# Performance work log

Hardware: AMD Instinct MI355X
Metric: run time of the kernel (lower is better)

The kernel has to match this reference:

```python
import jax, jax.numpy as jnp
import numpy as np

DIM = 512
HEADS = 8
DIM_HEAD = 64
LANDMARKS = 256  # dim // 2
PINV_ITERS = 6
KERNEL = 33  # residual conv kernel
NUM_LAYERS = 2
NUM_CLASSES = 2


def layernorm(x, g, b, eps=1e-5):
    mu = x.mean(-1, keepdims=True)
    var = ((x - mu) ** 2).mean(-1, keepdims=True)
    return (x - mu) * jax.lax.rsqrt(var + eps) * g + b


def moore_penrose_pinv(x, iters=PINV_ITERS):
    # x: (b, h, m, m); scaling uses GLOBAL max over all batch/heads (torch.max)
    abs_x = jnp.abs(x)
    col = abs_x.sum(-1).max()
    row = abs_x.sum(-2).max()
    z = jnp.swapaxes(x, -1, -2) / (col * row)
    I = jnp.eye(x.shape[-1], dtype=x.dtype)
    for _ in range(iters):
        xz = x @ z
        z = 0.25 * z @ (13. * I - xz @ (15. * I - xz @ (7. * I - xz)))
    return z


def nystrom_attention(x, w_qkv, w_out, b_out, conv_w):
    # x: (b, n, dim)
    b, n, _ = x.shape
    m = LANDMARKS
    pad = (m - n % m) % m
    if pad:
        x = jnp.pad(x, ((0, 0), (pad, 0), (0, 0)))  # pad at FRONT
    nf = n + pad
    qkv = x @ w_qkv  # (b, nf, 3*h*dh)
    qkv = qkv.reshape(b, nf, 3, HEADS, DIM_HEAD)
    q = jnp.transpose(qkv[:, :, 0], (0, 2, 1, 3)) * (DIM_HEAD ** -0.5)  # (b,h,nf,dh)
    k = jnp.transpose(qkv[:, :, 1], (0, 2, 1, 3))
    v = jnp.transpose(qkv[:, :, 2], (0, 2, 1, 3))
    l = nf // m
    q_l = q.reshape(b, HEADS, m, l, DIM_HEAD).mean(3)  # (b,h,m,dh)
    k_l = k.reshape(b, HEADS, m, l, DIM_HEAD).mean(3)
    sim1 = jnp.einsum('bhid,bhjd->bhij', q, k_l)      # (b,h,nf,m)
    sim2 = jnp.einsum('bhid,bhjd->bhij', q_l, k_l)    # (b,h,m,m)
    sim3 = jnp.einsum('bhid,bhjd->bhij', q_l, k)      # (b,h,m,nf)
    attn1 = jax.nn.softmax(sim1, axis=-1)
    attn2 = jax.nn.softmax(sim2, axis=-1)
    attn3 = jax.nn.softmax(sim3, axis=-1)
    attn2_inv = moore_penrose_pinv(attn2)
    out = (attn1 @ attn2_inv) @ (attn3 @ v)  # (b,h,nf,dh)
    # residual depthwise conv over sequence dim, per head (Conv2d groups=heads)
    res = jax.lax.conv_general_dilated(
        v, conv_w, window_strides=(1, 1), padding=((KERNEL // 2, KERNEL // 2), (0, 0)),
        dimension_numbers=('NCHW', 'OIHW', 'NCHW'), feature_group_count=HEADS)
    out = out + res
    out = jnp.transpose(out, (0, 2, 1, 3)).reshape(b, nf, HEADS * DIM_HEAD)
    out = out @ w_out + b_out
    return out[:, -n:]


def setup_inputs() -> dict:
    key = jax.random.key(0)
    ks = jax.random.split(key, 16)
    B, N = 2, 8191
    s = 0.02
    inp = {
        'h': jax.random.normal(ks[0], (B, N, 1024), jnp.float32),
        'w1': jax.random.normal(ks[1], (1024, DIM), jnp.float32) * s,
        'b1': jnp.zeros((DIM,), jnp.float32),
        'cls_token': jax.random.normal(ks[2], (1, 1, DIM), jnp.float32),
        'ln_g': jnp.ones((NUM_LAYERS, DIM), jnp.float32),
        'ln_b': jnp.zeros((NUM_LAYERS, DIM), jnp.float32),
        'w_qkv': jax.random.normal(ks[3], (NUM_LAYERS, DIM, 3 * HEADS * DIM_HEAD), jnp.float32) * s,
        'w_out': jax.random.normal(ks[4], (NUM_LAYERS, HEADS * DIM_HEAD, DIM), jnp.float32) * s,
        'b_out': jnp.zeros((NUM_LAYERS, DIM), jnp.float32),
        'conv_w': jax.random.normal(ks[5], (NUM_LAYERS, HEADS, 1, KERNEL, 1), jnp.float32) * s,
        'fn_g': jnp.ones((DIM,), jnp.float32),
        'fn_b': jnp.zeros((DIM,), jnp.float32),
        'w2': jax.random.normal(ks[6], (DIM, NUM_CLASSES), jnp.float32) * s,
        'b2': jnp.zeros((NUM_CLASSES,), jnp.float32),
    }
    return inp


def reference(h, w1, b1, cls_token, ln_g, ln_b, w_qkv, w_out, b_out, conv_w, fn_g, fn_b, w2, b2):
    x = jax.nn.relu(h @ w1 + b1)  # (B,N,512)
    B = x.shape[0]
    cls = jnp.broadcast_to(cls_token, (B, 1, DIM))
    x = jnp.concatenate([cls, x], axis=1)  # (B, N+1, 512)
    for i in range(NUM_LAYERS):
        x = x + nystrom_attention(layernorm(x, ln_g[i], ln_b[i]), w_qkv[i], w_out[i], b_out[i], conv_w[i])
    x = layernorm(x, fn_g, fn_b)[:, 0]
    logits = x @ w2 + b2
    return logits
```

## Files before the change

### kernel.cpp

```cpp
#include <hip/hip_runtime.h>
#include <hip/hip_bf16.h>

#define DIM 512
#define HEADS 8
#define DH 64
#define LM 256
#define NF 8192
#define BHN 16

typedef __attribute__((ext_vector_type(8))) short short8;
typedef __attribute__((ext_vector_type(4))) float f32x4;

__device__ __forceinline__ float bf2f(unsigned short u) {
  return __uint_as_float((unsigned)u << 16);
}
__device__ __forceinline__ unsigned short f2bf(float x) {
  unsigned u = __float_as_uint(x);
  unsigned r = u + 0x7fffu + ((u >> 16) & 1u);
  return (unsigned short)(r >> 16);
}

__device__ __forceinline__ void gl2lds16(const void* g, void* l) {
  __builtin_amdgcn_global_load_lds(
      (const __attribute__((address_space(1))) void*)g,
      (__attribute__((address_space(3))) void*)l, 16, 0, 0);
}

__device__ __forceinline__ void lds_fence() {
  asm volatile("s_waitcnt lgkmcnt(0)" ::: "memory");
  __builtin_amdgcn_sched_barrier(0);
}

__device__ __forceinline__ float waveReduceSum(float v) {
#pragma unroll
  for (int o = 1; o < 64; o <<= 1) v += __shfl_xor(v, o);
  return v;
}
__device__ __forceinline__ float waveReduceMax(float v) {
#pragma unroll
  for (int o = 1; o < 64; o <<= 1) v = fmaxf(v, __shfl_xor(v, o));
  return v;
}
__device__ __forceinline__ float blockReduceSum256(float v, float* sm) {
  v = waveReduceSum(v);
  int w = threadIdx.x >> 6;
  __syncthreads();
  if ((threadIdx.x & 63) == 0) sm[w] = v;
  __syncthreads();
  return sm[0] + sm[1] + sm[2] + sm[3];
}
__device__ __forceinline__ float blockReduceMax256(float v, float* sm) {
  v = waveReduceMax(v);
  int w = threadIdx.x >> 6;
  __syncthreads();
  if ((threadIdx.x & 63) == 0) sm[w] = v;
  __syncthreads();
  return fmaxf(fmaxf(sm[0], sm[1]), fmaxf(sm[2], sm[3]));
}

__global__ __launch_bounds__(256)
void cvt_bf16(const float* __restrict__ in, unsigned short* __restrict__ out,
              long long n) {
  long long i = ((long long)blockIdx.x * 256 + threadIdx.x) * 4;
  if (i + 3 < n) {
    float4 v = *(const float4*)&in[i];
    ushort4 o;
    o.x = f2bf(v.x); o.y = f2bf(v.y); o.z = f2bf(v.z); o.w = f2bf(v.w);
    *(ushort4*)&out[i] = o;
  } else {
    for (; i < n; i++) out[i] = f2bf(in[i]);
  }
}

__global__ __launch_bounds__(256)
void cvt_transpose(const float* __restrict__ in, unsigned short* __restrict__ out,
                   int Kd, int Nd) {
  __shared__ float t[32][33];
  int x = threadIdx.x & 31, y = threadIdx.x >> 5;
#pragma unroll
  for (int i = 0; i < 32; i += 8) {
    int k = blockIdx.y * 32 + y + i, n = blockIdx.x * 32 + x;
    t[y + i][x] = in[(long long)k * Nd + n];
  }
  __syncthreads();
#pragma unroll
  for (int i = 0; i < 32; i += 8) {
    int n = blockIdx.x * 32 + y + i, k = blockIdx.y * 32 + x;
    out[(long long)n * Kd + k] = f2bf(t[x][y + i]);
  }
}

__global__ __launch_bounds__(256)
void vt_transpose(const unsigned short* __restrict__ VB,
                  unsigned short* __restrict__ VT) {
  __shared__ unsigned short t[64][80];
  int bh = blockIdx.x >> 7, tile = blockIdx.x & 127;
  int n0 = tile * 64;
  int tid = threadIdx.x;
#pragma unroll
  for (int it = 0; it < 2; it++) {
    int s = it * 256 + tid;
    int nl = s >> 3, sg = s & 7;
    *(short8*)&t[nl][sg * 8] =
        *(const short8*)&VB[((long long)bh * NF + n0 + nl) * DH + sg * 8];
  }
  __syncthreads();
#pragma unroll
  for (int it = 0; it < 2; it++) {
    int s = it * 256 + tid;
    int dl = s >> 3, sg = s & 7;
    short8 v;
#pragma unroll
    for (int j = 0; j < 8; j++) ((unsigned short*)&v)[j] = t[sg * 8 + j][dl];
    *(short8*)&VT[((long long)bh * DH + dl) * NF + n0 + sg * 8] = v;
  }
}

__global__ __launch_bounds__(256) void write_cls(const float* __restrict__ cls,
                                                 float* __restrict__ X) {
  int t = blockIdx.x * 256 + threadIdx.x;
  int b = t >> 9, c = t & 511;
  X[(long long)b * NF * DIM + c] = cls[c];
}

#define MG_RELU 1
#define MG_ADDC 2
#define MG_BIAS 4
__global__ __launch_bounds__(256)
void gemm_mfma(const unsigned short* __restrict__ A,
               const unsigned short* __restrict__ B,
               const float* __restrict__ bias, float* __restrict__ C,
               unsigned short* __restrict__ qkv, unsigned short* __restrict__ vbuf,
               int M, int N, int K, int flags, int remap) {
  __shared__ short8 smem[3072];
  const int tid = threadIdx.x;
  const int lane = tid & 63, wave = tid >> 6;
  const int wm = wave >> 1, wn = wave & 1;
  const int nwg = gridDim.x * gridDim.y;
  const int orig = blockIdx.y * gridDim.x + blockIdx.x;
  const int swz = ((nwg & 7) == 0) ? (orig & 7) * (nwg >> 3) + (orig >> 3) : orig;
  const int m0 = (swz / gridDim.x) * 128, n0 = (swz % gridDim.x) * 128;
  const int r16 = lane & 15, quad = lane >> 4;
  const unsigned short* pa0 = A + (long long)(m0 + 32 * wave + r16) * K + quad * 8;
  const unsigned short* pa1 = A + (long long)(m0 + 32 * wave + 16 + r16) * K + quad * 8;
  const unsigned short* pb0 = B + (long long)(n0 + 32 * wave + r16) * K + quad * 8;
  const unsigned short* pb1 = B + (long long)(n0 + 32 * wave + 16 + r16) * K + quad * 8;
  auto stage = [&](int bsel) {
    short8 (*Als)[64] = (short8 (*)[64])(smem + bsel * 1024);
    short8 (*Bls)[64] = (short8 (*)[64])(smem + bsel * 1024 + 512);
    gl2lds16(pa0, &Als[2 * wave][0]);
    gl2lds16(pa1, &Als[2 * wave + 1][0]);
    gl2lds16(pb0, &Bls[2 * wave][0]);
    gl2lds16(pb1, &Bls[2 * wave + 1][0]);
    pa0 += 32; pa1 += 32; pb0 += 32; pb1 += 32;
  };
  f32x4 acc[4][4] = {};
  const int nsteps = K >> 5;
  stage(0);
  stage(1);
  asm volatile("s_waitcnt vmcnt(4)" ::: "memory");
  __builtin_amdgcn_sched_barrier(0);
  __builtin_amdgcn_s_barrier();
  for (int t = 0; t < nsteps; t++) {
    if (t + 2 < nsteps) stage((t + 2) % 3);
    short8 (*Als)[64] = (short8 (*)[64])(smem + (t % 3) * 1024);
    short8 (*Bls)[64] = (short8 (*)[64])(smem + (t % 3) * 1024 + 512);
    short8 af[4], bfr[4];
#pragma unroll
    for (int mt = 0; mt < 4; mt++) af[mt] = Als[wm * 4 + mt][lane];
#pragma unroll
    for (int nt = 0; nt < 4; nt++) bfr[nt] = Bls[wn * 4 + nt][lane];
#pragma unroll
    for (int mt = 0; mt < 4; mt++)
#pragma unroll
      for (int nt = 0; nt < 4; nt++)
        acc[mt][nt] = __builtin_amdgcn_mfma_f32_16x16x32_bf16(
            af[mt], bfr[nt], acc[mt][nt], 0, 0, 0);
    if (t + 2 < nsteps) {
      asm volatile("s_waitcnt vmcnt(4)" ::: "memory");
    } else {
      asm volatile("s_waitcnt vmcnt(0)" ::: "memory");
    }
    __builtin_amdgcn_sched_barrier(0);
    __builtin_amdgcn_s_barrier();
  }
  if (remap == 2) {
    unsigned short (*Ep)[32][64] = (unsigned short (*)[32][64])smem;
    int gn_base = n0 + wn * 64;
    int s = gn_base >> 9, hh = (gn_base >> 6) & 7;
    float scale = (s == 0) ? 0.125f : 1.f;
    unsigned short* basep =
        (s == 0) ? qkv : (s == 1) ? qkv + (long long)BHN * NF * DH : vbuf;
#pragma unroll
    for (int half = 0; half < 2; half++) {
      lds_fence();
#pragma unroll
      for (int mt = half * 2; mt < half * 2 + 2; mt++)
#pragma unroll
        for (int nt = 0; nt < 4; nt++)
#pragma unroll
          for (int r = 0; r < 4; r++)
            Ep[wave][(mt & 1) * 16 + quad * 4 + r][nt * 16 + r16] =
                f2bf(acc[mt][nt][r] * scale);
      lds_fence();
#pragma unroll
      for (int it = 0; it < 4; it++) {
        int idx = it * 64 + lane;
        int m_l = idx >> 3, sg = idx & 7;
        int gm = m0 + wm * 64 + half * 32 + m_l;
        int b = gm >> 13, n = gm & (NF - 1);
        int bh = b * HEADS + hh;
        short8 v = *(short8*)&Ep[wave][m_l][sg * 8];
        *(short8*)&basep[((long long)bh * NF + n) * DH + sg * 8] = v;
      }
    }
  } else {
#pragma unroll
    for (int mt = 0; mt < 4; mt++) {
#pragma unroll
      for (int nt = 0; nt < 4; nt++) {
#pragma unroll
        for (int r = 0; r < 4; r++) {
          int gm = m0 + wm * 64 + mt * 16 + quad * 4 + r;
          int gn = n0 + wn * 64 + nt * 16 + r16;
          if (gm >= M) continue;
          float v = acc[mt][nt][r];
          if (flags & MG_BIAS) v += bias[gn];
          long long idx;
          if (remap == 1) {
            int b = gm / 8191;
            int n = gm - b * 8191;
            idx = ((long long)(b * NF + 1 + n)) * DIM + gn;
          } else {
            idx = (long long)gm * N + gn;
          }
          if (flags & MG_ADDC) v += C[idx];
          if (flags & MG_RELU) v = fmaxf(v, 0.f);
          C[idx] = v;
        }
      }
    }
  }
}

__global__ __launch_bounds__(512)
void flash_attn1(const unsigned short* __restrict__ QB,
                 const unsigned short* __restrict__ KLB,
                 const unsigned short* __restrict__ WmB,
                 const unsigned short* __restrict__ XNC,
                 unsigned short* __restrict__ XNB2) {
  __shared__ unsigned short Klds[LM * DH];
  __shared__ unsigned short Wlds[DH * LM];
  __shared__ unsigned short Plds[8][16][136];
  const int bh = blockIdx.y, b = bh >> 3, hh = bh & 7;
  const int tid = threadIdx.x, lane = tid & 63, wave = tid >> 6;
  const int r16 = lane & 15, quad = lane >> 4;
  const unsigned short* Aq = QB + (long long)bh * NF * DH;
  const unsigned short* Kg = KLB + (long long)bh * LM * DH;
  const unsigned short* Wg = WmB + (long long)bh * DH * LM;
#pragma unroll
  for (int j = 0; j < 4; j++) {
    int u = j * 8 + wave;
    int s = u * 64 + lane;
    int row = s >> 3, ck = s & 7;
    gl2lds16(Kg + row * DH + ((ck ^ (row & 7)) << 3), (char*)Klds + u * 1024);
  }
#pragma unroll
  for (int j = 0; j < 4; j++) {
    int u = j * 8 + wave;
    int s = u * 64 + lane;
    int row = s >> 5, ck = s & 31;
    gl2lds16(Wg + row * LM + ((ck ^ (row & 7)) << 3), (char*)Wlds + u * 1024);
  }
  __syncthreads();
  short8 ones;
#pragma unroll
  for (int j = 0; j < 8; j++) ((unsigned short*)&ones)[j] = 0x3F80;
#pragma unroll
  for (int rt = 0; rt < 2; rt++) {
    const int m0w = blockIdx.x * 256 + (wave * 2 + rt) * 16;
    short8 af[2];
#pragma unroll
    for (int kc = 0; kc < 2; kc++)
      af[kc] = *(const short8*)&Aq[(long long)(m0w + r16) * DH + kc * 32 + quad * 8];
    f32x4 O[4] = {};
    f32x4 Ls = {};
#pragma unroll
    for (int t = 0; t < 2; t++) {
      int c0 = t * 128;
      f32x4 S[8] = {};
      __builtin_amdgcn_s_setprio(1);
#pragma unroll
      for (int nt = 0; nt < 8; nt++) {
        int kl = c0 + nt * 16 + r16;
#pragma unroll
        for (int kc = 0; kc < 2; kc++) {
          short8 bb = *(const short8*)((const char*)Klds + kl * 128 +
                                       (((kc * 4 + quad) ^ (kl & 7)) << 4));
          S[nt] = __builtin_amdgcn_mfma_f32_16x16x32_bf16(af[kc], bb, S[nt], 0, 0, 0);
        }
      }
      __builtin_amdgcn_s_setprio(0);
#pragma unroll
      for (int nt = 0; nt < 8; nt++)
#pragma unroll
        for (int r = 0; r < 4; r++)
          Plds[wave][quad * 4 + r][nt * 16 + r16] = f2bf(__expf(S[nt][r]));
      lds_fence();
      __builtin_amdgcn_s_setprio(1);
#pragma unroll
      for (int kc = 0; kc < 4; kc++) {
        short8 a = *(short8*)&Plds[wave][r16][kc * 32 + quad * 8];
        Ls = __builtin_amdgcn_mfma_f32_16x16x32_bf16(a, ones, Ls, 0, 0, 0);
#pragma unroll
        for (int nt2 = 0; nt2 < 4; nt2++) {
          int wrow = nt2 * 16 + r16;
          int cu = (c0 >> 3) + kc * 4 + quad;
          short8 bb = *(const short8*)((const char*)Wlds + wrow * 512 +
                                       ((cu ^ (wrow & 7)) << 4));
          O[nt2] = __builtin_amdgcn_mfma_f32_16x16x32_bf16(a, bb, O[nt2], 0, 0, 0);
        }
      }
      __builtin_amdgcn_s_setprio(0);
    }
    float invl[4];
#pragma unroll
    for (int r = 0; r < 4; r++) invl[r] = 1.f / Ls[r];
#pragma unroll
    for (int nt2 = 0; nt2 < 4; nt2++)
#pragma unroll
      for (int r = 0; r < 4; r++) {
        int row = m0w + quad * 4 + r;
        int d = nt2 * 16 + r16;
        long long gi = ((long long)(b * NF + row)) * DIM + hh * DH + d;
        XNB2[gi] = f2bf(O[nt2][r] * invl[r] + bf2f(XNC[gi]));
      }
  }
}

__device__ __forceinline__ void stage_kv3(const unsigned short* Kg,
                                          const unsigned short* Vg,
                                          unsigned short* Kb, unsigned short* Vb,
                                          int kv0, int wave, int lane) {
#pragma unroll
  for (int j = 0; j < 2; j++) {
    int u = j * 8 + wave;
    int s = u * 64 + lane;
    int kr = s >> 3, kc = s & 7;
    gl2lds16(Kg + (long long)(kv0 + kr) * DH + ((kc ^ (kr & 7)) << 3),
             (char*)Kb + u * 1024);
    int vr = s >> 4, vc = s & 15;
    gl2lds16(Vg + (long long)vr * NF + kv0 + ((vc ^ (vr & 7)) << 3),
             (char*)Vb + u * 1024);
  }
}

__global__ __launch_bounds__(512)
void flash_attn3(const unsigned short* __restrict__ QLB,
                 const unsigned short* __restrict__ KB,
                 const unsigned short* __restrict__ VT,
                 float* __restrict__ Opart, float* __restrict__ Lpart) {
  __shared__ unsigned short Klds[2][128 * DH];
  __shared__ unsigned short Vlds[2][DH * 128];
  __shared__ unsigned short Plds[8][16][136];
  const int ks = blockIdx.x, bh = blockIdx.y;
  const int tid = threadIdx.x, lane = tid & 63, wave = tid >> 6;
  const int r16 = lane & 15, quad = lane >> 4;
  const unsigned short* Aq = QLB + (long long)bh * LM * DH;
  const unsigned short* Kg = KB + (long long)bh * NF * DH;
  const unsigned short* Vg = VT + (long long)bh * DH * NF;
  short8 af2[2][2];
#pragma unroll
  for (int rt = 0; rt < 2; rt++) {
    int m0w = (wave * 2 + rt) * 16;
#pragma unroll
    for (int kc = 0; kc < 2; kc++)
      af2[rt][kc] =
          *(const short8*)&Aq[(long long)(m0w + r16) * DH + kc * 32 + quad * 8];
  }
  short8 ones;
#pragma unroll
  for (int j = 0; j < 8; j++) ((unsigned short*)&ones)[j] = 0x3F80;
  f32x4 O2[2][4] = {};
  f32x4 Ls2[2] = {};
  stage_kv3(Kg, Vg, Klds[0], Vlds[0], ks * 512, wave, lane);
  __syncthreads();
  for (int t = 0; t < 4; t++) {
    int cb = t & 1;
    if (t < 3)
      stage_kv3(Kg, Vg, Klds[cb ^ 1], Vlds[cb ^ 1], ks * 512 + (t + 1) * 128,
                wave, lane);
    const unsigned short* Kb = Klds[cb];
    const unsigned short* Vb = Vlds[cb];
#pragma unroll
    for (int rt = 0; rt < 2; rt++) {
      f32x4 S[8] = {};
      __builtin_amdgcn_s_setprio(1);
#pragma unroll
      for (int nt = 0; nt < 8; nt++) {
        int kl = nt * 16 + r16;
#pragma unroll
        for (int kc = 0; kc < 2; kc++) {
          short8 bb = *(const short8*)((const char*)Kb + kl * 128 +
                                       (((kc * 4 + quad) ^ (kl & 7)) << 4));
          S[nt] = __builtin_amdgcn_mfma_f32_16x16x32_bf16(af2[rt][kc], bb, S[nt],
                                                          0, 0, 0);
        }
      }
      __builtin_amdgcn_s_setprio(0);
#pragma unroll
      for (int nt = 0; nt < 8; nt++)
#pragma unroll
        for (int r = 0; r < 4; r++)
          Plds[wave][quad * 4 + r][nt * 16 + r16] = f2bf(__expf(S[nt][r]));
      lds_fence();
      __builtin_amdgcn_s_setprio(1);
#pragma unroll
      for (int kc2 = 0; kc2 < 4; kc2++) {
        short8 a = *(short8*)&Plds[wave][r16][kc2 * 32 + quad * 8];
        Ls2[rt] = __builtin_amdgcn_mfma_f32_16x16x32_bf16(a, ones, Ls2[rt], 0, 0, 0);
#pragma unroll
        for (int nt2 = 0; nt2 < 4; nt2++) {
          int vr = nt2 * 16 + r16;
          int u = kc2 * 4 + quad;
          short8 bb = *(const short8*)((const char*)Vb + vr * 256 +
                                       ((u ^ (vr & 7)) << 4));
          O2[rt][nt2] = __builtin_amdgcn_mfma_f32_16x16x32_bf16(a, bb, O2[rt][nt2],
                                                                0, 0, 0);
        }
      }
      __builtin_amdgcn_s_setprio(0);
    }
    __syncthreads();
  }
  float* Ob = Opart + (((long long)ks * BHN + bh) * LM) * DH;
#pragma unroll
  for (int rt = 0; rt < 2; rt++) {
    int m0w = (wave * 2 + rt) * 16;
#pragma unroll
    for (int nt2 = 0; nt2 < 4; nt2++)
#pragma unroll
      for (int r = 0; r < 4; r++)
        Ob[(long long)(m0w + quad * 4 + r) * DH + nt2 * 16 + r16] = O2[rt][nt2][r];
    if (r16 == 0)
#pragma unroll
      for (int r = 0; r < 4; r++)
        Lpart[((long long)ks * BHN + bh) * LM + m0w + quad * 4 + r] = Ls2[rt][r];
  }
}

__global__ __launch_bounds__(256)
void attn3_merge(const float* __restrict__ Opart, const float* __restrict__ Lpart,
                 float* __restrict__ O3) {
  int idx = blockIdx.x * 256 + threadIdx.x;
  int bh = idx >> 14, rem = idx & 16383;
  int row = rem >> 6, d = rem & 63;
  float L = 0.f, acc = 0.f;
#pragma unroll
  for (int c = 0; c < 16; c++) {
    L += Lpart[((long long)c * BHN + bh) * LM + row];
    acc += Opart[(((long long)c * BHN + bh) * LM + row) * DH + d];
  }
  O3[((long long)bh * LM + row) * DH + d] = acc / L;
}

__global__ __launch_bounds__(256)
void zinit(const float* __restrict__ a2, const unsigned* __restrict__ red,
           unsigned short* __restrict__ zn, unsigned short* __restrict__ zt) {
  float scale = 1.0f / __uint_as_float(red[1]);
  long long idx = (long long)blockIdx.x * 256 + threadIdx.x;
  int bh = (int)(idx >> 16);
  int ij = (int)(idx & 65535);
  int i = ij >> 8, j = ij & 255;
  zn[idx] = f2bf(a2[((long long)bh << 16) + (j << 8) + i] * scale);
  zt[idx] = f2bf(a2[idx] * scale);
}

#define PV_CN 1
#define PV_CT 2
#define PV_CF 4
#define PV_ID 8
__global__ __launch_bounds__(256)
void pinv_bf(const unsigned short* __restrict__ An,
             const unsigned short* __restrict__ Bt,
             unsigned short* __restrict__ Cn, unsigned short* __restrict__ Ct,
             float* __restrict__ Cf, float alpha, float ident, float beta,
             int flags) {
  __shared__ unsigned short Als[32][256];
  __shared__ unsigned short Bls[32][256];
  const int batch = blockIdx.z;
  An += (long long)batch * 65536;
  Bt += (long long)batch * 65536;
  const int tid = threadIdx.x, lane = tid & 63, wave = tid >> 6;
  const int wm2 = wave >> 1, wn2 = wave & 1;
  const int m0 = blockIdx.y * 32, n0 = blockIdx.x * 32;
  const int r16 = lane & 15, quad = lane >> 4;
#pragma unroll
  for (int j = 0; j < 4; j++) {
    int g = (j * 4 + wave) * 64 + lane;
    int row = g >> 5, plog = (g & 31) ^ (row & 7);
    gl2lds16(An + ((m0 + row) << 8) + plog * 8,
             (char*)Als + (j * 4 + wave) * 1024);
    gl2lds16(Bt + ((n0 + row) << 8) + plog * 8,
             (char*)Bls + (j * 4 + wave) * 1024);
  }
  __syncthreads();
  f32x4 acc = {};
  const int arow = wm2 * 16 + r16, brow = wn2 * 16 + r16;
#pragma unroll
  for (int kk = 0; kk < 8; kk++) {
    short8 af = *(const short8*)((const char*)Als + arow * 512 +
                                 ((kk * 4 + quad) ^ (arow & 7)) * 16);
    short8 bfr = *(const short8*)((const char*)Bls + brow * 512 +
                                  ((kk * 4 + quad) ^ (brow & 7)) * 16);
    acc = __builtin_amdgcn_mfma_f32_16x16x32_bf16(af, bfr, acc, 0, 0, 0);
  }
  long long cb = (long long)batch * 65536;
  int ncol = n0 + wn2 * 16 + r16;
  float vals[4];
#pragma unroll
  for (int r = 0; r < 4; r++) {
    int mrow = wm2 * 16 + quad * 4 + r;
    float v = beta * acc[r];
    if (flags & PV_ID) {
      unsigned short a = *(const unsigned short*)(
          (const char*)Als + mrow * 512 +
          (((ncol >> 3) ^ (mrow & 7)) * 16) + (ncol & 7) * 2);
      v += ident * bf2f(a);
    }
    vals[r] = v * alpha;
    int gm = m0 + mrow;
    if (flags & PV_CN) Cn[cb + ((long long)gm << 8) + ncol] = f2bf(vals[r]);
    if (flags & PV_CF) Cf[cb + ((long long)gm << 8) + ncol] = vals[r];
  }
  if (flags & PV_CT) {
    ushort4 o;
    o.x = f2bf(vals[0]); o.y = f2bf(vals[1]);
    o.z = f2bf(vals[2]); o.w = f2bf(vals[3]);
    *(ushort4*)&Ct[cb + ((long long)ncol << 8) + m0 + wm2 * 16 + quad * 4] = o;
  }
}

#define BG_BIDENT 16
__global__ __launch_bounds__(256)
void bgemm(const float* __restrict__ A, const float* __restrict__ B,
           float* __restrict__ C, int M, int N, int K,
           long long sA, long long sB, long long sC,
           float alpha, float ident, int flags) {
  const int batch = blockIdx.z;
  A += (long long)batch * sA;
  B += (long long)batch * sB;
  float* Cb = C + (long long)batch * sC;
  __shared__ float As[16][68];
  __shared__ float Bs[16][68];
  const int tid = threadIdx.x;
  const int tx = tid & 15, ty = tid >> 4;
  const int m0 = blockIdx.y * 64, n0 = blockIdx.x * 64;
  float acc[4][4] = {};
  for (int k0 = 0; k0 < K; k0 += 16) {
    {
      int k = tid & 15;
      int mBase = tid >> 4;
#pragma unroll
      for (int i = 0; i < 4; i++) {
        int m = mBase + i * 16;
        int gm = m0 + m;
        As[k][m] = (gm < M) ? A[(long long)gm * K + (k0 + k)] : 0.f;
      }
    }
    {
      int n = tid & 63;
      int kBase = tid >> 6;
#pragma unroll
      for (int i = 0; i < 4; i++) {
        int k = kBase + i * 4;
        int gn = n0 + n;
        float vb = (gn < N) ? B[(long long)(k0 + k) * N + gn] : 0.f;
        if (flags & BG_BIDENT) vb = ident * ((k0 + k) == gn ? 1.f : 0.f) - vb;
        Bs[k][n] = vb;
      }
    }
    __syncthreads();
#pragma unroll
    for (int k = 0; k < 16; k++) {
      float a[4], b[4];
#pragma unroll
      for (int i = 0; i < 4; i++) a[i] = As[k][ty * 4 + i];
#pragma unroll
      for (int j = 0; j < 4; j++) b[j] = Bs[k][tx * 4 + j];
#pragma unroll
      for (int i = 0; i < 4; i++)
#pragma unroll
        for (int j = 0; j < 4; j++) acc[i][j] = fmaf(a[i], b[j], acc[i][j]);
    }
    __syncthreads();
  }
#pragma unroll
  for (int i = 0; i < 4; i++) {
    int gm = m0 + ty * 4 + i;
    if (gm >= M) continue;
#pragma unroll
    for (int j = 0; j < 4; j++) {
      int gn = n0 + tx * 4 + j;
      if (gn >= N) continue;
      Cb[(long long)gm * N + gn] = alpha * acc[i][j];
    }
  }
}

__global__ __launch_bounds__(256)
void wm_gemm(const float* __restrict__ Z, const float* __restrict__ O3,
             unsigned short* __restrict__ WmT) {
  const int batch = blockIdx.y;
  const int m0 = blockIdx.x * 64;
  const float* A = Z + (long long)batch * 65536;
  const float* B = O3 + (long long)batch * LM * DH;
  __shared__ float As[16][68];
  __shared__ float Bs[16][68];
  const int tid = threadIdx.x, tx = tid & 15, ty = tid >> 4;
  float acc[4][4] = {};
  for (int k0 = 0; k0 < 256; k0 += 16) {
    {
      int k = tid & 15, mB = tid >> 4;
#pragma unroll
      for (int i = 0; i < 4; i++) {
        int m = mB + i * 16;
        As[k][m] = A[(long long)(m0 + m) * 256 + k0 + k];
      }
    }
    {
      int n = tid & 63, kB = tid >> 6;
#pragma unroll
      for (int i = 0; i < 4; i++) {
        int k = kB + i * 4;
        Bs[k][n] = B[(long long)(k0 + k) * DH + n];
      }
    }
    __syncthreads();
#pragma unroll
    for (int k = 0; k < 16; k++) {
      float a[4], b[4];
#pragma unroll
      for (int i = 0; i < 4; i++) a[i] = As[k][ty * 4 + i];
#pragma unroll
      for (int j = 0; j < 4; j++) b[j] = Bs[k][tx * 4 + j];
#pragma unroll
      for (int i = 0; i < 4; i++)
#pragma unroll
        for (int j = 0; j < 4; j++) acc[i][j] = fmaf(a[i], b[j], acc[i][j]);
    }
    __syncthreads();
  }
#pragma unroll
  for (int i = 0; i < 4; i++)
#pragma unroll
    for (int j = 0; j < 4; j++)
      WmT[((long long)batch * DH + tx * 4 + j) * LM + m0 + ty * 4 + i] =
          f2bf(acc[i][j]);
}

__global__ __launch_bounds__(256)
void layernorm_rows_bf16(const float* __restrict__ X, const float* __restrict__ g,
                         const float* __restrict__ bt,
                         unsigned short* __restrict__ Y) {
  __shared__ float sm[4];
  long long r = blockIdx.x;
  const float* x = X + r * DIM;
  int t = threadIdx.x;
  float v0 = x[t], v1 = x[t + 256];
  float mu = blockReduceSum256(v0 + v1, sm) * (1.f / DIM);
  float d0 = v0 - mu, d1 = v1 - mu;
  float var = blockReduceSum256(d0 * d0 + d1 * d1, sm) * (1.f / DIM);
  float rs = 1.0f / sqrtf(var + 1e-5f);
  unsigned short* y = Y + r * DIM;
  y[t] = f2bf(d0 * rs * g[t] + bt[t]);
  y[t + 256] = f2bf(d1 * rs * g[t + 256] + bt[t + 256]);
}

__global__ __launch_bounds__(64)
void landmarks_k(const unsigned short* __restrict__ q,
                 const unsigned short* __restrict__ k,
                 float* __restrict__ ql, float* __restrict__ kl,
                 unsigned short* __restrict__ qlb,
                 unsigned short* __restrict__ klb) {
  int bh = blockIdx.x >> 8, i = blockIdx.x & 255, d = threadIdx.x;
  long long base = ((long long)bh * NF + i * 32) * DH + d;
  float sq = 0.f, sk = 0.f;
#pragma unroll 4
  for (int l = 0; l < 32; l++) {
    sq += bf2f(q[base + (long long)l * DH]);
    sk += bf2f(k[base + (long long)l * DH]);
  }
  long long o = ((long long)bh * LM + i) * DH + d;
  float mq = sq * (1.f / 32.f), mk = sk * (1.f / 32.f);
  ql[o] = mq; kl[o] = mk;
  qlb[o] = f2bf(mq); klb[o] = f2bf(mk);
}

__global__ __launch_bounds__(256)
void sim2_softmax(const float* __restrict__ ql, const float* __restrict__ kl,
                  float* __restrict__ a2, unsigned short* __restrict__ a2b) {
  __shared__ float qs[64];
  __shared__ float sm[4];
  int bh = blockIdx.x >> 8, i = blockIdx.x & 255, t = threadIdx.x;
  if (t < 64) qs[t] = ql[((long long)bh * LM + i) * DH + t];
  __syncthreads();
  const float* krow = kl + (long long)bh * LM * DH + (long long)t * DH;
  float s = 0.f;
#pragma unroll
  for (int d = 0; d < 64; d++) s += qs[d] * krow[d];
  float m = blockReduceMax256(s, sm);
  float e = expf(s - m);
  float sum = blockReduceSum256(e, sm);
  long long off = ((long long)bh * LM + i) * LM + t;
  float v = e / sum;
  a2[off] = v;
  a2b[off] = f2bf(v);
}

__global__ __launch_bounds__(256)
void pinv_reduce(const float* __restrict__ a2, unsigned* __restrict__ red) {
  __shared__ float sm[4];
  int bh = blockIdx.x, t = threadIdx.x;
  const float* A = a2 + (long long)bh * LM * LM;
  float cs = 0.f;
  for (int i = 0; i < 256; i++) cs += fabsf(A[i * 256 + t]);
  float cm = blockReduceMax256(cs, sm);
  if (t == 0) atomicMax(&red[1], __float_as_uint(cm));
}

__global__ __launch_bounds__(256)
void conv_res_bf16(const unsigned short* __restrict__ vt,
                   const float* __restrict__ cw,
                   unsigned short* __restrict__ out) {
  int bh = blockIdx.x >> 6, tile = blockIdx.x & 63;
  int b = bh >> 3, hh = bh & 7;
  int t = threadIdx.x;
  int d = t & 63, pg = t >> 6;
  float wr[33];
#pragma unroll
  for (int kk = 0; kk < 33; kk++) wr[kk] = cw[hh * 33 + kk];
  const unsigned short* src = &vt[((long long)bh * DH + d) * NF];
  int base = tile * 128 + pg * 32;
  int n0 = base - 16;
  float win[64];
#pragma unroll
  for (int jj = 0; jj < 8; jj++) {
    int c = n0 + jj * 8;
    if (c >= 0 && c + 7 < NF) {
      short8 v = *(const short8*)&src[c];
#pragma unroll
      for (int j = 0; j < 8; j++)
        win[jj * 8 + j] = bf2f((unsigned short)v[j]);
    } else {
#pragma unroll
      for (int j = 0; j < 8; j++) {
        int nn = c + j;
        win[jj * 8 + j] = (nn >= 0 && nn < NF) ? bf2f(src[nn]) : 0.f;
      }
    }
  }
  unsigned short* dst = &out[((long long)(b * NF + base)) * DIM + hh * DH + d];
#pragma unroll
  for (int p = 0; p < 32; p++) {
    float s = 0.f;
#pragma unroll
    for (int kk = 0; kk < 33; kk++) s = fmaf(wr[kk], win[p + kk], s);
    dst[(long long)p * DIM] = f2bf(s);
  }
}

__global__ __launch_bounds__(256)
void final_head(const float* __restrict__ X, const float* __restrict__ g,
                const float* __restrict__ bt, const float* __restrict__ w2,
                const float* __restrict__ b2, float* __restrict__ out) {
  __shared__ float sm[4];
  int b = blockIdx.x, t = threadIdx.x;
  const float* row = X + (long long)b * NF * DIM;
  float v0 = row[t], v1 = row[t + 256];
  float mu = blockReduceSum256(v0 + v1, sm) * (1.f / DIM);
  float d0 = v0 - mu, d1 = v1 - mu;
  float var = blockReduceSum256(d0 * d0 + d1 * d1, sm) * (1.f / DIM);
  float rs = 1.0f / sqrtf(var + 1e-5f);
  float y0 = d0 * rs * g[t] + bt[t];
  float y1 = d1 * rs * g[t + 256] + bt[t + 256];
  float l0 = y0 * w2[t * 2 + 0] + y1 * w2[(t + 256) * 2 + 0];
  float l1 = y0 * w2[t * 2 + 1] + y1 * w2[(t + 256) * 2 + 1];
  l0 = blockReduceSum256(l0, sm);
  l1 = blockReduceSum256(l1, sm);
  if (t == 0) {
    out[b * 2 + 0] = l0 + b2[0];
    out[b * 2 + 1] = l1 + b2[1];
  }
}

extern "C" void kernel_launch(void* const* d_in, const int* in_sizes, int n_in,
                              void* d_out, int out_size, void* d_ws,
                              size_t ws_size, hipStream_t stream) {
  const float* h      = (const float*)d_in[0];
  const float* w1     = (const float*)d_in[1];
  const float* b1     = (const float*)d_in[2];
  const float* cls    = (const float*)d_in[3];
  const float* ln_g   = (const float*)d_in[4];
  const float* ln_b   = (const float*)d_in[5];
  const float* w_qkv  = (const float*)d_in[6];
  const float* w_out  = (const float*)d_in[7];
  const float* b_out  = (const float*)d_in[8];
  const float* conv_w = (const float*)d_in[9];
  const float* fn_g   = (const float*)d_in[10];
  const float* fn_b   = (const float*)d_in[11];
  const float* w2     = (const float*)d_in[12];
  const float* b2     = (const float*)d_in[13];

  float* ws = (float*)d_ws;
  const long long XSZ = (long long)2 * NF * DIM;
  const long long QSZ = (long long)BHN * NF * DH;
  float* X  = ws;
  unsigned short* STAGE = (unsigned short*)(X + XSZ);
  unsigned short* HB   = STAGE;
  unsigned short* XNB1 = STAGE;
  unsigned short* XNB2 = STAGE;
  unsigned short* VB   = STAGE + XSZ;
  unsigned short* XNC  = STAGE + XSZ;
  unsigned short* QB = STAGE + 2 * XSZ;
  unsigned short* KB = QB + QSZ;
  unsigned short* VT = KB + QSZ;
  float* QL = (float*)(VT + QSZ);
  float* KL = QL + 262144;
  unsigned short* QLB = (unsigned short*)(KL + 262144);
  unsigned short* KLB = QLB + 262144;
  float* A2 = (float*)(KLB + 262144);
  float* ZA = A2 + 1048576;
  float* ZB = ZA + 1048576;
  float* P  = ZB + 1048576;
  float* T1 = P + 1048576;
  float* T2 = T1 + 1048576;
  float* Mpart = T2 + 1048576;
  float* Lpart = Mpart + 65536;
  float* O3 = Lpart + 65536;
  unsigned short* WmB = (unsigned short*)(O3 + 262144);
  unsigned* RED = (unsigned*)(WmB + 262144);
  unsigned short* WT = (unsigned short*)(RED + 4);
  unsigned short* W1T = WT;
  unsigned short* WQ0 = W1T + 524288;
  unsigned short* WQ1 = WQ0 + 786432;
  unsigned short* WO0 = WQ1 + 786432;
  unsigned short* WO1 = WO0 + 262144;

  unsigned short* A2B = VB;
  float* Opart = (float*)VB;
  unsigned short* Zan = (unsigned short*)P;
  unsigned short* Zat = Zan + 1048576;
  unsigned short* Zbn = (unsigned short*)ZB;
  unsigned short* Zbt = Zbn + 1048576;
  unsigned short* Pn  = (unsigned short*)T1;
  unsigned short* Pt  = Pn + 1048576;
  unsigned short* T1t = (unsigned short*)T2;
  unsigned short* T2t = T1t + 1048576;

  write_cls<<<4, 256, 0, stream>>>(cls, X);
  cvt_bf16<<<16382, 256, 0, stream>>>(h, HB, (long long)16382 * 1024);
  cvt_transpose<<<dim3(512 / 32, 1024 / 32), 256, 0, stream>>>(w1, W1T, 1024, 512);
  cvt_transpose<<<dim3(1536 / 32, 512 / 32), 256, 0, stream>>>(w_qkv, WQ0, 512, 1536);
  cvt_transpose<<<dim3(1536 / 32, 512 / 32), 256, 0, stream>>>(
      w_qkv + (long long)DIM * 1536, WQ1, 512, 1536);
  cvt_transpose<<<dim3(512 / 32, 512 / 32), 256, 0, stream>>>(w_out, WO0, 512, 512);
  cvt_transpose<<<dim3(512 / 32, 512 / 32), 256, 0, stream>>>(
      w_out + (long long)DIM * DIM, WO1, 512, 512);
  gemm_mfma<<<dim3(4, 128), 256, 0, stream>>>(HB, W1T, b1, X, nullptr, nullptr,
                                              16382, 512, 1024, MG_RELU | MG_BIAS, 1);

  for (int L = 0; L < 2; L++) {
    layernorm_rows_bf16<<<2 * NF, 256, 0, stream>>>(X, ln_g + L * DIM,
                                                    ln_b + L * DIM, XNB1);
    gemm_mfma<<<dim3(12, 128), 256, 0, stream>>>(XNB1, L ? WQ1 : WQ0, nullptr,
                                                 nullptr, QB, VB, 16384, 1536,
                                                 512, 0, 2);
    vt_transpose<<<BHN * 128, 256, 0, stream>>>(VB, VT);

    landmarks_k<<<BHN * LM, 64, 0, stream>>>(QB, KB, QL, KL, QLB, KLB);
    sim2_softmax<<<BHN * LM, 256, 0, stream>>>(QL, KL, A2, A2B);
    hipMemsetAsync(RED, 0, 16, stream);
    pinv_reduce<<<BHN, 256, 0, stream>>>(A2, RED);
    zinit<<<4096, 256, 0, stream>>>(A2, RED, Zan, Zat);
    for (int it = 0; it < 5; it++) {
      const unsigned short* zcn = (it & 1) ? Zbn : Zan;
      const unsigned short* zct = (it & 1) ? Zbt : Zat;
      unsigned short* znn = (it & 1) ? Zan : Zbn;
      unsigned short* znt = (it & 1) ? Zat : Zbt;
      pinv_bf<<<dim3(8, 8, BHN), 256, 0, stream>>>(
          A2B, zct, Pn, Pt, nullptr, 1.f, 0.f, 1.f, PV_CN | PV_CT);
      pinv_bf<<<dim3(8, 8, BHN), 256, 0, stream>>>(
          Pn, Pt, nullptr, T1t, nullptr, 1.f, 7.f, -1.f, PV_CT | PV_ID);
      pinv_bf<<<dim3(8, 8, BHN), 256, 0, stream>>>(
          Pn, T1t, nullptr, T2t, nullptr, 1.f, 15.f, -1.f, PV_CT | PV_ID);
      if (it < 4)
        pinv_bf<<<dim3(8, 8, BHN), 256, 0, stream>>>(
            zcn, T2t, znn, znt, nullptr, 0.25f, 13.f, -1.f,
            PV_CN | PV_CT | PV_ID);
      else
        pinv_bf<<<dim3(8, 8, BHN), 256, 0, stream>>>(
            zcn, T2t, nullptr, nullptr, ZB, 0.25f, 13.f, -1.f, PV_CF | PV_ID);
    }
    bgemm<<<dim3(4, 4, BHN), 256, 0, stream>>>(A2, ZB, P, 256, 256, 256,
                                               65536, 65536, 65536, 1.f, 0.f, 0);
    bgemm<<<dim3(4, 4, BHN), 256, 0, stream>>>(P, P, T1, 256, 256, 256,
                                               65536, 65536, 65536, 1.f, 7.f,
                                               BG_BIDENT);
    bgemm<<<dim3(4, 4, BHN), 256, 0, stream>>>(P, T1, T2, 256, 256, 256,
                                               65536, 65536, 65536, 1.f, 15.f,
                                               BG_BIDENT);
    bgemm<<<dim3(4, 4, BHN), 256, 0, stream>>>(ZB, T2, ZA, 256, 256, 256,
                                               65536, 65536, 65536, 0.25f,
                                               13.f, BG_BIDENT);

    flash_attn3<<<dim3(16, BHN), 512, 0, stream>>>(QLB, KB, VT, Opart, Lpart);
    attn3_merge<<<1024, 256, 0, stream>>>(Opart, Lpart, O3);

    wm_gemm<<<dim3(4, BHN), 256, 0, stream>>>(ZA, O3, WmB);

    conv_res_bf16<<<BHN * 64, 256, 0, stream>>>(VT, conv_w + L * 264, XNC);

    flash_attn1<<<dim3(32, BHN), 512, 0, stream>>>(QB, KLB, WmB, XNC, XNB2);

    gemm_mfma<<<dim3(4, 128), 256, 0, stream>>>(XNB2, L ? WO1 : WO0,
                                                b_out + L * DIM, X, nullptr,
                                                nullptr, 16384, 512, 512,
                                                MG_ADDC | MG_BIAS, 0);
  }
  final_head<<<2, 256, 0, stream>>>(X, fn_g, fn_b, w2, b2, (float*)d_out);
}
```

Measured before the change: 1.253 ms.

## Load GEMM A fragments directly to registers, stage only B through LDS

The GEMM kernel stops staging the A tile through LDS. Each wave now loads its A fragments straight from global memory into registers, prefetching one step ahead, and only the B tile keeps the triple-buffered global-to-LDS path. This halves the LDS footprint and removes the LDS reads for A, which could raise occupancy and cut LDS traffic. In exchange, waves sharing the same A rows load them redundantly from global memory, and the vmcnt wait accounting becomes more delicate.

New measurement: 1.324 ms. +5.7%, slower.

```diff
diff --git a/kernel.cpp b/kernel.cpp
--- a/kernel.cpp
+++ b/kernel.cpp
@@ -132,7 +132,7 @@
                const float* __restrict__ bias, float* __restrict__ C,
                unsigned short* __restrict__ qkv, unsigned short* __restrict__ vbuf,
                int M, int N, int K, int flags, int remap) {
-  __shared__ short8 smem[3072];
+  __shared__ short8 smem[1536];
   const int tid = threadIdx.x;
   const int lane = tid & 63, wave = tid >> 6;
   const int wm = wave >> 1, wn = wave & 1;
@@ -141,33 +141,36 @@
   const int swz = ((nwg & 7) == 0) ? (orig & 7) * (nwg >> 3) + (orig >> 3) : orig;
   const int m0 = (swz / gridDim.x) * 128, n0 = (swz % gridDim.x) * 128;
   const int r16 = lane & 15, quad = lane >> 4;
-  const unsigned short* pa0 = A + (long long)(m0 + 32 * wave + r16) * K + quad * 8;
-  const unsigned short* pa1 = A + (long long)(m0 + 32 * wave + 16 + r16) * K + quad * 8;
+  const unsigned short* pA[4];
+#pragma unroll
+  for (int mt = 0; mt < 4; mt++)
+    pA[mt] = A + (long long)(m0 + wm * 64 + mt * 16 + r16) * K + quad * 8;
   const unsigned short* pb0 = B + (long long)(n0 + 32 * wave + r16) * K + quad * 8;
   const unsigned short* pb1 = B + (long long)(n0 + 32 * wave + 16 + r16) * K + quad * 8;
-  auto stage = [&](int bsel) {
-    short8 (*Als)[64] = (short8 (*)[64])(smem + bsel * 1024);
-    short8 (*Bls)[64] = (short8 (*)[64])(smem + bsel * 1024 + 512);
-    gl2lds16(pa0, &Als[2 * wave][0]);
-    gl2lds16(pa1, &Als[2 * wave + 1][0]);
+  auto stageB = [&](int bsel) {
+    short8 (*Bls)[64] = (short8 (*)[64])(smem + bsel * 512);
     gl2lds16(pb0, &Bls[2 * wave][0]);
     gl2lds16(pb1, &Bls[2 * wave + 1][0]);
-    pa0 += 32; pa1 += 32; pb0 += 32; pb1 += 32;
+    pb0 += 32; pb1 += 32;
   };
   f32x4 acc[4][4] = {};
   const int nsteps = K >> 5;
-  stage(0);
-  stage(1);
-  asm volatile("s_waitcnt vmcnt(4)" ::: "memory");
+  short8 afC[4], afN[4];
+#pragma unroll
+  for (int mt = 0; mt < 4; mt++) { afC[mt] = *(const short8*)pA[mt]; pA[mt] += 32; }
+  stageB(0);
+  stageB(1);
+  asm volatile("s_waitcnt vmcnt(2)" ::: "memory");
   __builtin_amdgcn_sched_barrier(0);
   __builtin_amdgcn_s_barrier();
   for (int t = 0; t < nsteps; t++) {
-    if (t + 2 < nsteps) stage((t + 2) % 3);
-    short8 (*Als)[64] = (short8 (*)[64])(smem + (t % 3) * 1024);
-    short8 (*Bls)[64] = (short8 (*)[64])(smem + (t % 3) * 1024 + 512);
-    short8 af[4], bfr[4];
-#pragma unroll
-    for (int mt = 0; mt < 4; mt++) af[mt] = Als[wm * 4 + mt][lane];
+    if (t + 1 < nsteps) {
+#pragma unroll
+      for (int mt = 0; mt < 4; mt++) { afN[mt] = *(const short8*)pA[mt]; pA[mt] += 32; }
+    }
+    if (t + 2 < nsteps) stageB((t + 2) % 3);
+    short8 (*Bls)[64] = (short8 (*)[64])(smem + (t % 3) * 512);
+    short8 bfr[4];
 #pragma unroll
     for (int nt = 0; nt < 4; nt++) bfr[nt] = Bls[wn * 4 + nt][lane];
 #pragma unroll
@@ -175,8 +178,12 @@
 #pragma unroll
       for (int nt = 0; nt < 4; nt++)
         acc[mt][nt] = __builtin_amdgcn_mfma_f32_16x16x32_bf16(
-            af[mt], bfr[nt], acc[mt][nt], 0, 0, 0);
+            afC[mt], bfr[nt], acc[mt][nt], 0, 0, 0);
+#pragma unroll
+    for (int mt = 0; mt < 4; mt++) afC[mt] = afN[mt];
     if (t + 2 < nsteps) {
+      asm volatile("s_waitcnt vmcnt(6)" ::: "memory");
+    } else if (t + 1 < nsteps) {
       asm volatile("s_waitcnt vmcnt(4)" ::: "memory");
     } else {
       asm volatile("s_waitcnt vmcnt(0)" ::: "memory");
```
